# Optimization experiments

Hardware: AMD Instinct MI355X
Metric: run time of the kernel (lower is better)

## Reference

```python
import jax, jax.numpy as jnp
import numpy as np

B, T, D, H, LAT = 64, 512, 128, 512, 128


def setup_inputs() -> dict:
    key = jax.random.key(0)
    ks = jax.random.split(key, 17)
    s = lambda k, shape: (jax.random.normal(k, shape, jnp.float32) * 0.05)
    return {
        "padded_input": jax.random.normal(ks[0], (B, T, D), jnp.float32),
        "lengths": jnp.full((B,), T, jnp.int32),  # full lengths: packed == padded
        "W_ih_f": s(ks[1], (4 * H, D)), "W_hh_f": s(ks[2], (4 * H, H)), "b_f": s(ks[3], (4 * H,)),
        "W_ih_b": s(ks[4], (4 * H, D)), "W_hh_b": s(ks[5], (4 * H, H)), "b_b": s(ks[6], (4 * H,)),
        "W_ih_d": s(ks[7], (4 * H, D)), "W_hh_d": s(ks[8], (4 * H, H)), "b_d": s(ks[9], (4 * H,)),
        "W_lat": s(ks[10], (LAT, 4 * H)), "b_lat": s(ks[11], (LAT,)),
        "W_l2h": s(ks[12], (H, LAT)), "b_l2h": s(ks[13], (H,)),
        "W_out": s(ks[14], (D, H)), "b_out": s(ks[15], (D,)),
        "skip_alpha": jnp.asarray(0.5, jnp.float32),
    }


def _lstm(x, W_ih, W_hh, b, h0, c0):
    # x: [B, T, Din]; PyTorch gate order i, f, g, o; b = b_ih + b_hh pre-summed.
    xg = jnp.einsum('btd,gd->tbg', x, W_ih) + b  # [T, B, 4H], input GEMM hoisted out of scan

    def step(carry, xg_t):
        h, c = carry
        g = xg_t + h @ W_hh.T
        i, f, gc, o = jnp.split(g, 4, axis=-1)
        c = jax.nn.sigmoid(f) * c + jax.nn.sigmoid(i) * jnp.tanh(gc)
        h = jax.nn.sigmoid(o) * jnp.tanh(c)
        return (h, c), h

    (hT, cT), ys = jax.lax.scan(step, (h0, c0), xg)
    return jnp.transpose(ys, (1, 0, 2)), hT, cT  # [B, T, H], final h, final c


def reference(padded_input, lengths, W_ih_f, W_hh_f, b_f, W_ih_b, W_hh_b, b_b,
              W_ih_d, W_hh_d, b_d, W_lat, b_lat, W_l2h, b_l2h, W_out, b_out, skip_alpha):
    Bz, Tz, _ = padded_input.shape
    dt = padded_input.dtype
    z0 = jnp.zeros((Bz, H), dt)

    # Bidirectional encoder (single layer)
    out_f, hf, _ = _lstm(padded_input, W_ih_f, W_hh_f, b_f, z0, z0)
    out_b_rev, hb, _ = _lstm(padded_input[:, ::-1, :], W_ih_b, W_hh_b, b_b, z0, z0)
    out_b = out_b_rev[:, ::-1, :]
    enc_out = jnp.concatenate([out_f, out_b], axis=-1)  # [B, T, 2H]
    h_cat = jnp.concatenate([hf, hb], axis=-1)          # [B, 2H]

    # Masked mean pooling over valid timesteps
    mask = (jnp.arange(Tz)[None, :] < lengths[:, None]).astype(dt)[..., None]
    mean_hidden = (enc_out * mask).sum(axis=1) / lengths[:, None].astype(dt)
    latent_input = jnp.concatenate([h_cat, mean_hidden], axis=-1)  # [B, 4H]
    latent = latent_input @ W_lat.T + b_lat

    # Decoder init from latent; c0 = zeros
    h_dec = latent @ W_l2h.T + b_l2h

    # Teacher forcing with ratio 1.0, eval dropout, no noise:
    # per-step loop == one LSTM over padded_input[:, :T-1]
    dec_in = padded_input[:, :Tz - 1, :]
    y, _, _ = _lstm(dec_in, W_ih_d, W_hh_d, b_d, h_dec, jnp.zeros_like(h_dec))
    decoded = jnp.einsum('bth,dh->btd', y, W_out) + b_out  # [B, T-1, D]

    alpha = jax.nn.sigmoid(skip_alpha)
    return alpha * decoded + (1.0 - alpha) * padded_input[:, 1:, :]
```

## Files before the change

### kernel.cpp

```cpp
#include <hip/hip_runtime.h>
#include <cstdint>
#include <cstddef>

typedef __attribute__((ext_vector_type(8))) short bf16x8;
typedef __attribute__((ext_vector_type(4))) float f32x4;
typedef __attribute__((ext_vector_type(4))) unsigned u32x4;
typedef __attribute__((ext_vector_type(2))) unsigned u32x2;
typedef unsigned short ushort_t;

constexpr int kB = 64;
constexpr int kT = 512;
constexpr int kD = 128;
constexpr int kH = 512;
constexpr int kLat = 128;

constexpr size_t OFF_Y   = 0;
constexpr size_t Y_EL    = (size_t)(kT - 1) * kH * kB;
constexpr size_t OFF_XBF = OFF_Y + Y_EL;
constexpr size_t XBF_F   = (size_t)kT * kB * kD / 2;
constexpr size_t OFF_HT  = OFF_XBF + XBF_F;
constexpr size_t HT_F    = 3 * 2 * 32768 / 2;
constexpr size_t OFF_RDY = OFF_HT + HT_F;
constexpr size_t RDY_I   = 3 * 512 * 32;
constexpr size_t OFF_HFF = OFF_RDY + RDY_I;
constexpr size_t OFF_HFB = OFF_HFF + 32768;
constexpr size_t OFF_HSF = OFF_HFB + 32768;
constexpr size_t OFF_HSB = OFF_HSF + 32768;
constexpr size_t NEED_BYTES = (OFF_HSB + 32768) * 4;

#define MFMA_B16(A, Bv, C) C = __builtin_amdgcn_mfma_f32_16x16x32_bf16(A, Bv, C, 0, 0, 0)

__device__ __forceinline__ float sigf(float x) { return 1.0f / (1.0f + __expf(-x)); }
__device__ __forceinline__ float tanh_(float x) {
  float xc = fminf(fmaxf(x, -15.f), 15.f);
  float e = __expf(2.f * xc);
  return (e - 1.f) / (e + 1.f);
}
__device__ __forceinline__ ushort_t f2bf(float f) {
  unsigned u = __float_as_uint(f);
  u = (u + 0x7FFFu + ((u >> 16) & 1u)) >> 16;
  return (ushort_t)u;
}
__device__ __forceinline__ bf16x8 pack8(float4 a, float4 b) {
  bf16x8 v;
  v[0] = (short)f2bf(a.x); v[1] = (short)f2bf(a.y);
  v[2] = (short)f2bf(a.z); v[3] = (short)f2bf(a.w);
  v[4] = (short)f2bf(b.x); v[5] = (short)f2bf(b.y);
  v[6] = (short)f2bf(b.z); v[7] = (short)f2bf(b.w);
  return v;
}
__device__ __forceinline__ float cellup(const f32x4 a, float& c) {
  float ig = sigf(a[0]), fg = sigf(a[1]), gg = tanh_(a[2]), og = sigf(a[3]);
  c = fg * c + ig * gg;
  return og * tanh_(c);
}

__device__ __forceinline__ u32x4 llc_load_b128(const void* p) {
  u32x4 v;
  asm volatile("global_load_dwordx4 %0, %1, off sc0 sc1"
               : "=v"(v) : "v"(p) : "memory");
  return v;
}
__device__ __forceinline__ void llc_store_b64(void* p, u32x2 v) {
  asm volatile("global_store_dwordx2 %0, %1, off sc0 sc1"
               :: "v"(p), "v"(v) : "memory");
}
__device__ __forceinline__ void llc_store_b32(void* p, unsigned v) {
  asm volatile("global_store_dword %0, %1, off sc0 sc1"
               :: "v"(p), "v"(v) : "memory");
}
__device__ __forceinline__ void wait_vm0() {
  asm volatile("s_waitcnt vmcnt(0)" ::: "memory");
  __builtin_amdgcn_sched_barrier(0);
}

__global__ __launch_bounds__(256) void xbf_k(const float* __restrict__ X,
                                             ushort_t* __restrict__ xbf) {
  const int t = blockIdx.x, tid = threadIdx.x;
  const int b = tid >> 2, dq = (tid & 3) * 32;
  const float* src = X + ((size_t)b * kT + t) * kD + dq;
  ushort_t* dst = xbf + ((size_t)t * kB + b) * kD + dq;
  #pragma unroll
  for (int i = 0; i < 32; i += 8) {
    float4 u0 = *(const float4*)(src + i);
    float4 u1 = *(const float4*)(src + i + 4);
    *(bf16x8*)(dst + i) = pack8(u0, u1);
  }
}

__device__ __forceinline__ void xproj(const ushort_t* xb0, int q, const bf16x8* Ax,
                                      f32x4& a0, f32x4& a1, f32x4& a2, f32x4& a3,
                                      int b0n, int b1n, int b2n, int b3n) {
  #pragma unroll
  for (int ks = 0; ks < 4; ++ks) {
    const int ko = ks * 32 + q * 8;
    bf16x8 x0 = *(const bf16x8*)(xb0 + b0n * 128 + ko);
    bf16x8 x1 = *(const bf16x8*)(xb0 + b1n * 128 + ko);
    bf16x8 x2 = *(const bf16x8*)(xb0 + b2n * 128 + ko);
    bf16x8 x3 = *(const bf16x8*)(xb0 + b3n * 128 + ko);
    MFMA_B16(Ax[ks], x0, a0);
    MFMA_B16(Ax[ks], x1, a1);
    MFMA_B16(Ax[ks], x2, a2);
    MFMA_B16(Ax[ks], x3, a3);
  }
}

template<int MODE>
__global__ __launch_bounds__(256, 1) void lstm_k(
    const float* __restrict__ WhhA, const float* __restrict__ WhhB,
    const float* __restrict__ WihA, const float* __restrict__ WihB,
    const float* __restrict__ biaA, const float* __restrict__ biaB,
    const int* __restrict__ lengths, const ushort_t* __restrict__ xbf,
    float* __restrict__ ws) {
  __shared__ ushort_t hlds[32768];
  __shared__ ushort_t hx[64 * 20];
  const int tid = threadIdx.x;
  const int bid = blockIdx.x;
  const bool fwd = (MODE == 1) ? true : (bid < 32);
  const int gl = (MODE == 1) ? bid : (bid & 31);
  const float* Whh = fwd ? WhhA : WhhB;
  const float* Wih = fwd ? WihA : WihB;
  const float* bia = fwd ? biaA : biaB;
  const int dir_off = (MODE == 1) ? 2 : (fwd ? 0 : 1);
  ushort_t* hT = (ushort_t*)(ws + OFF_HT) + dir_off * 65536;
  unsigned* rdyf = (unsigned*)(ws + OFF_RDY) + (size_t)dir_off * 512 * 32;
  const int TS = (MODE == 1) ? (kT - 1) : kT;

  const int w = tid >> 6, lane = tid & 63;
  const int q = lane >> 4, r = lane & 15;
  const int JB = gl * 16;
  const int j4 = JB + 4 * w;
  const int gate = r & 3, jj = j4 + (r >> 2);

  bf16x8 Ah[16], Ax[4];
  {
    const float* p = Whh + ((size_t)(gate * kH + jj)) * kH + q * 8;
    #pragma unroll
    for (int ks = 0; ks < 16; ++ks)
      Ah[ks] = pack8(*(const float4*)(p + ks * 32), *(const float4*)(p + ks * 32 + 4));
    const float* px = Wih + ((size_t)(gate * kH + jj)) * kD + q * 8;
    #pragma unroll
    for (int ks = 0; ks < 4; ++ks)
      Ax[ks] = pack8(*(const float4*)(px + ks * 32), *(const float4*)(px + ks * 32 + 4));
  }
  const int jq = j4 + q;
  f32x4 bias_v;
  bias_v[0] = bia[0 * kH + jq];
  bias_v[1] = bia[1 * kH + jq];
  bias_v[2] = bia[2 * kH + jq];
  bias_v[3] = bia[3 * kH + jq];
  const int b0n = r, b1n = 16 + r, b2n = 32 + r, b3n = 48 + r;
  int len0 = 0, len1 = 0, len2 = 0, len3 = 0;
  if (MODE == 0) {
    len0 = lengths[b0n]; len1 = lengths[b1n];
    len2 = lengths[b2n]; len3 = lengths[b3n];
  }
  float c0 = 0.f, c1 = 0.f, c2 = 0.f, c3 = 0.f;
  float hs0 = 0.f, hs1 = 0.f, hs2 = 0.f, hs3 = 0.f;
  f32x4 a0 = bias_v, a1 = bias_v, a2 = bias_v, a3 = bias_v;
  {
    const int tx = fwd ? 0 : (kT - 1);
    xproj(xbf + (size_t)tx * 8192, q, Ax, a0, a1, a2, a3, b0n, b1n, b2n, b3n);
  }
  char* lp = (char*)hlds;
  float* yout = ws + OFF_Y;

  for (int t = 0; t < TS; ++t) {
    if (t > 0) {
      if (w == 0) {
        const unsigned* fp = rdyf + (size_t)t * 32 + (lane & 31);
        for (;;) {
          unsigned v = __hip_atomic_load(fp, __ATOMIC_RELAXED, __HIP_MEMORY_SCOPE_AGENT);
          if (__ballot(v != 0u) == ~0ull) break;
          __builtin_amdgcn_s_sleep(1);
        }
        __builtin_amdgcn_sched_barrier(0);
      }
      __syncthreads();
    }
    {
      const char* hsrc = (const char*)(hT + (t & 1) * 32768);
      u32x4 reg[16];
      #pragma unroll
      for (int i = 0; i < 16; ++i) {
        const int idx = tid + i * 256;
        reg[i] = llc_load_b128(hsrc + (size_t)idx * 16);
      }
      wait_vm0();
      #pragma unroll
      for (int i = 0; i < 16; ++i) {
        const int idx = tid + i * 256;
        const int bb = idx >> 6, cc = idx & 63;
        *(u32x4*)(lp + (((bb << 10) + (cc << 4)) ^ ((bb & 7) << 4))) = reg[i];
      }
    }
    __syncthreads();
    #pragma unroll
    for (int ks = 0; ks < 16; ++ks) {
      const int kb = ks * 64 + (q << 4);
      bf16x8 v0 = *(const bf16x8*)(lp + (((b0n << 10) + kb) ^ ((b0n & 7) << 4)));
      bf16x8 v1 = *(const bf16x8*)(lp + (((b1n << 10) + kb) ^ ((b1n & 7) << 4)));
      bf16x8 v2 = *(const bf16x8*)(lp + (((b2n << 10) + kb) ^ ((b2n & 7) << 4)));
      bf16x8 v3 = *(const bf16x8*)(lp + (((b3n << 10) + kb) ^ ((b3n & 7) << 4)));
      MFMA_B16(Ah[ks], v0, a0);
      MFMA_B16(Ah[ks], v1, a1);
      MFMA_B16(Ah[ks], v2, a2);
      MFMA_B16(Ah[ks], v3, a3);
    }
    const float h0v = cellup(a0, c0);
    const float h1v = cellup(a1, c1);
    const float h2v = cellup(a2, c2);
    const float h3v = cellup(a3, c3);
    if (MODE == 0) {
      const bool m0 = fwd ? (t < len0) : (t >= kT - len0);
      const bool m1 = fwd ? (t < len1) : (t >= kT - len1);
      const bool m2 = fwd ? (t < len2) : (t >= kT - len2);
      const bool m3 = fwd ? (t < len3) : (t >= kT - len3);
      hs0 += m0 ? h0v : 0.f;
      hs1 += m1 ? h1v : 0.f;
      hs2 += m2 ? h2v : 0.f;
      hs3 += m3 ? h3v : 0.f;
    } else {
      yout[((size_t)t * kH + jq) * kB + b0n] = h0v;
      yout[((size_t)t * kH + jq) * kB + b1n] = h1v;
      yout[((size_t)t * kH + jq) * kB + b2n] = h2v;
      yout[((size_t)t * kH + jq) * kB + b3n] = h3v;
    }
    if (t < TS - 1) {
      const int jl = 4 * w + q;
      hx[b0n * 20 + jl] = f2bf(h0v);
      hx[b1n * 20 + jl] = f2bf(h1v);
      hx[b2n * 20 + jl] = f2bf(h2v);
      hx[b3n * 20 + jl] = f2bf(h3v);
      __syncthreads();
      {
        const int bb = tid >> 2, c4 = (tid & 3) * 4;
        u32x2 v = *(const u32x2*)&hx[bb * 20 + c4];
        llc_store_b64(hT + ((t + 1) & 1) * 32768 + bb * 512 + JB + c4, v);
      }
      __syncthreads();
      if (tid == 0) llc_store_b32(rdyf + (size_t)(t + 1) * 32 + gl, 1u);
      a0 = bias_v; a1 = bias_v; a2 = bias_v; a3 = bias_v;
      const int tx = fwd ? (t + 1) : (kT - 1 - (t + 1));
      xproj(xbf + (size_t)tx * 8192, q, Ax, a0, a1, a2, a3, b0n, b1n, b2n, b3n);
    } else if (MODE == 0) {
      float* hfin = ws + (fwd ? OFF_HFF : OFF_HFB);
      float* hsum = ws + (fwd ? OFF_HSF : OFF_HSB);
      hfin[jq * kB + b0n] = h0v; hfin[jq * kB + b1n] = h1v;
      hfin[jq * kB + b2n] = h2v; hfin[jq * kB + b3n] = h3v;
      hsum[jq * kB + b0n] = hs0; hsum[jq * kB + b1n] = hs1;
      hsum[jq * kB + b2n] = hs2; hsum[jq * kB + b3n] = hs3;
    }
  }
}

__global__ __launch_bounds__(256) void latent_k(
    const float* __restrict__ W_lat, const float* __restrict__ b_lat,
    const float* __restrict__ W_l2h, const float* __restrict__ b_l2h,
    const int* __restrict__ lengths, float* __restrict__ ws) {
  __shared__ __align__(16) float li[4 * kH];
  __shared__ __align__(16) float ls[kLat];
  const int b = blockIdx.x;
  const int tid = threadIdx.x;
  const float invlen = 1.0f / (float)lengths[b];
  for (int j = tid; j < kH; j += 256) {
    li[j]          = ws[OFF_HFF + (size_t)j * kB + b];
    li[kH + j]     = ws[OFF_HFB + (size_t)j * kB + b];
    li[2 * kH + j] = ws[OFF_HSF + (size_t)j * kB + b] * invlen;
    li[3 * kH + j] = ws[OFF_HSB + (size_t)j * kB + b] * invlen;
  }
  __syncthreads();
  if (tid < kLat) {
    const float* wv = W_lat + (size_t)tid * (4 * kH);
    float a = b_lat[tid];
    for (int k = 0; k < 4 * kH; k += 4) {
      const float4 w4 = *(const float4*)(wv + k);
      a += w4.x * li[k] + w4.y * li[k + 1] + w4.z * li[k + 2] + w4.w * li[k + 3];
    }
    ls[tid] = a;
  }
  __syncthreads();
  ushort_t* hTd = (ushort_t*)(ws + OFF_HT) + 2 * 65536;
  for (int j = tid; j < kH; j += 256) {
    const float* wv = W_l2h + (size_t)j * kLat;
    float a = b_l2h[j];
    #pragma unroll
    for (int k = 0; k < kLat; k += 4) {
      const float4 w4 = *(const float4*)(wv + k);
      a += w4.x * ls[k] + w4.y * ls[k + 1] + w4.z * ls[k + 2] + w4.w * ls[k + 3];
    }
    hTd[b * kH + j] = f2bf(a);
  }
}

__global__ __launch_bounds__(256) void out_k(
    const float* __restrict__ X, const float* __restrict__ W_out,
    const float* __restrict__ b_out, const float* __restrict__ alpha_p,
    const float* __restrict__ ws, float* __restrict__ out) {
  __shared__ __align__(16) float ys[128 * 64];
  __shared__ __align__(16) float Wo[128 * 128];
  const int t = blockIdx.x;
  const float* y = ws + OFF_Y + (size_t)t * kH * kB;
  const int tid = threadIdx.x;
  float acc[8][4];
  #pragma unroll
  for (int i = 0; i < 8; ++i)
    #pragma unroll
    for (int jj = 0; jj < 4; ++jj) acc[i][jj] = 0.f;
  const int tg = tid >> 4, tb = tid & 15;
  const int d0 = tg * 8, b0 = tb * 4;
  for (int ch = 0; ch < 4; ++ch) {
    __syncthreads();
    {
      const float4* s4 = (const float4*)(y + ch * 128 * 64);
      float4* d4 = (float4*)ys;
      #pragma unroll
      for (int i = 0; i < 8; ++i) d4[tid + i * 256] = s4[tid + i * 256];
    }
    {
      const int d = tid & 127, k0 = (tid >> 7) * 64;
      const float* src = W_out + (size_t)d * kH + ch * 128 + k0;
      #pragma unroll
      for (int i = 0; i < 64; i += 4) {
        float4 v = *(const float4*)(src + i);
        Wo[(k0 + i + 0) * 128 + d] = v.x;
        Wo[(k0 + i + 1) * 128 + d] = v.y;
        Wo[(k0 + i + 2) * 128 + d] = v.z;
        Wo[(k0 + i + 3) * 128 + d] = v.w;
      }
    }
    __syncthreads();
    #pragma unroll 2
    for (int k = 0; k < 128; ++k) {
      const float4 yv = *(const float4*)&ys[k * 64 + b0];
      const float4 w0 = *(const float4*)&Wo[k * 128 + d0];
      const float4 w1 = *(const float4*)&Wo[k * 128 + d0 + 4];
      const float wv[8] = {w0.x, w0.y, w0.z, w0.w, w1.x, w1.y, w1.z, w1.w};
      const float ya[4] = {yv.x, yv.y, yv.z, yv.w};
      #pragma unroll
      for (int di = 0; di < 8; ++di)
        #pragma unroll
        for (int bi = 0; bi < 4; ++bi)
          acc[di][bi] += wv[di] * ya[bi];
    }
  }
  const float alpha = sigf(alpha_p[0]);
  const float beta = 1.0f - alpha;
  #pragma unroll
  for (int bi = 0; bi < 4; ++bi) {
    const int b = b0 + bi;
    const float* xrow = X + ((size_t)b * kT + t + 1) * kD + d0;
    float* orow = out + ((size_t)b * (kT - 1) + t) * kD + d0;
    #pragma unroll
    for (int di = 0; di < 8; di += 4) {
      const float4 xv = *(const float4*)(xrow + di);
      float4 o;
      o.x = alpha * (acc[di + 0][bi] + b_out[d0 + di + 0]) + beta * xv.x;
      o.y = alpha * (acc[di + 1][bi] + b_out[d0 + di + 1]) + beta * xv.y;
      o.z = alpha * (acc[di + 2][bi] + b_out[d0 + di + 2]) + beta * xv.z;
      o.w = alpha * (acc[di + 3][bi] + b_out[d0 + di + 3]) + beta * xv.w;
      *(float4*)(orow + di) = o;
    }
  }
}

__global__ __launch_bounds__(256) void fallback_k(
    const float* __restrict__ X, const float* __restrict__ alpha_p,
    float* __restrict__ out, int n) {
  const int o = blockIdx.x * 256 + threadIdx.x;
  if (o >= n) return;
  const float alpha = sigf(alpha_p[0]);
  const int b = o / ((kT - 1) * kD);
  const int rr = o % ((kT - 1) * kD);
  const int t = rr / kD, d = rr % kD;
  out[o] = (1.0f - alpha) * X[((size_t)b * kT + t + 1) * kD + d];
}

extern "C" void kernel_launch(void* const* d_in, const int* in_sizes, int n_in,
                              void* d_out, int out_size, void* d_ws, size_t ws_size,
                              hipStream_t stream) {
  const float* X      = (const float*)d_in[0];
  const int*   lens   = (const int*)  d_in[1];
  const float* W_ih_f = (const float*)d_in[2];
  const float* W_hh_f = (const float*)d_in[3];
  const float* b_f    = (const float*)d_in[4];
  const float* W_ih_b = (const float*)d_in[5];
  const float* W_hh_b = (const float*)d_in[6];
  const float* b_b    = (const float*)d_in[7];
  const float* W_ih_d = (const float*)d_in[8];
  const float* W_hh_d = (const float*)d_in[9];
  const float* b_d    = (const float*)d_in[10];
  const float* W_lat  = (const float*)d_in[11];
  const float* b_lat  = (const float*)d_in[12];
  const float* W_l2h  = (const float*)d_in[13];
  const float* b_l2h  = (const float*)d_in[14];
  const float* W_out  = (const float*)d_in[15];
  const float* b_out  = (const float*)d_in[16];
  const float* alpha  = (const float*)d_in[17];
  float* ws  = (float*)d_ws;
  float* out = (float*)d_out;

  if (ws_size < NEED_BYTES) {
    fallback_k<<<(out_size + 255) / 256, 256, 0, stream>>>(X, alpha, out, out_size);
    return;
  }

  hipMemsetAsync((void*)(ws + OFF_HT), 0, (HT_F + RDY_I) * sizeof(float), stream);

  ushort_t* xbf = (ushort_t*)(ws + OFF_XBF);
  xbf_k<<<kT, 256, 0, stream>>>(X, xbf);
  lstm_k<0><<<64, 256, 0, stream>>>(W_hh_f, W_hh_b, W_ih_f, W_ih_b, b_f, b_b,
                                    lens, xbf, ws);
  latent_k<<<64, 256, 0, stream>>>(W_lat, b_lat, W_l2h, b_l2h, lens, ws);
  lstm_k<1><<<32, 256, 0, stream>>>(W_hh_d, nullptr, W_ih_d, nullptr, b_d, nullptr,
                                    lens, xbf, ws);
  out_k<<<kT - 1, 256, 0, stream>>>(X, W_out, b_out, alpha, ws, out);
}
```

Before: 5.603 ms.

## Replace global barrier wait with per-producer flag polling and early h publish

Each wave now polls only the readiness flags of the 8 producer blocks whose hidden-state slice it consumes, and copies each slice into LDS as soon as that producer is ready. This replaces the single wave-0 wait on all 32 flags followed by a bulk copy. The new hidden state is also published before the mask/accumulate or y-store work rather than after it, shortening the cross-block critical path. The cost is more polling traffic, an extra __syncthreads before reusing the hx buffer, and more complex per-wave control flow.

```diff
diff --git a/kernel.cpp b/kernel.cpp
--- a/kernel.cpp
+++ b/kernel.cpp
@@ -164,53 +164,82 @@
   }
   char* lp = (char*)hlds;
   float* yout = ws + OFF_Y;
+  const int p0 = 8 * w;
 
   for (int t = 0; t < TS; ++t) {
-    if (t > 0) {
-      if (w == 0) {
-        const unsigned* fp = rdyf + (size_t)t * 32 + (lane & 31);
-        for (;;) {
-          unsigned v = __hip_atomic_load(fp, __ATOMIC_RELAXED, __HIP_MEMORY_SCOPE_AGENT);
-          if (__ballot(v != 0u) == ~0ull) break;
-          __builtin_amdgcn_s_sleep(1);
+    const bool do_rec = (MODE == 1) || (t > 0);
+    if (do_rec) {
+      const ushort_t* hbase = hT + (t & 1) * 32768;
+      unsigned done = 0;
+      while (done != 0xFFu) {
+        unsigned todo;
+        if (MODE == 0 || t > 0) {
+          unsigned fl = 0;
+          if (lane < 8)
+            fl = __hip_atomic_load(rdyf + (size_t)t * 32 + p0 + lane,
+                                   __ATOMIC_RELAXED, __HIP_MEMORY_SCOPE_AGENT);
+          unsigned rdy8 = (unsigned)(__ballot(fl != 0u) & 0xFFull);
+          todo = rdy8 & ~done;
+          if (!todo) { __builtin_amdgcn_s_sleep(1); continue; }
+          __builtin_amdgcn_sched_barrier(0);
+        } else {
+          todo = 0xFFu;
         }
-        __builtin_amdgcn_sched_barrier(0);
+        u32x4 r0v[8], r1v[8];
+        #pragma unroll
+        for (int pi = 0; pi < 8; ++pi) {
+          if ((todo >> pi) & 1u) {
+            const ushort_t* src = hbase + lane * 512 + (p0 + pi) * 16;
+            r0v[pi] = llc_load_b128(src);
+            r1v[pi] = llc_load_b128(src + 8);
+          }
+        }
+        wait_vm0();
+        #pragma unroll
+        for (int pi = 0; pi < 8; ++pi) {
+          if ((todo >> pi) & 1u) {
+            const int pb = (p0 + pi) << 5;
+            *(u32x4*)(lp + (((lane << 10) + pb) ^ ((lane & 7) << 4))) = r0v[pi];
+            *(u32x4*)(lp + (((lane << 10) + pb + 16) ^ ((lane & 7) << 4))) = r1v[pi];
+          }
+        }
+        done |= todo;
       }
       __syncthreads();
-    }
-    {
-      const char* hsrc = (const char*)(hT + (t & 1) * 32768);
-      u32x4 reg[16];
       #pragma unroll
-      for (int i = 0; i < 16; ++i) {
-        const int idx = tid + i * 256;
-        reg[i] = llc_load_b128(hsrc + (size_t)idx * 16);
+      for (int ks = 0; ks < 16; ++ks) {
+        const int kb = ks * 64 + (q << 4);
+        bf16x8 v0 = *(const bf16x8*)(lp + (((b0n << 10) + kb) ^ ((b0n & 7) << 4)));
+        bf16x8 v1 = *(const bf16x8*)(lp + (((b1n << 10) + kb) ^ ((b1n & 7) << 4)));
+        bf16x8 v2 = *(const bf16x8*)(lp + (((b2n << 10) + kb) ^ ((b2n & 7) << 4)));
+        bf16x8 v3 = *(const bf16x8*)(lp + (((b3n << 10) + kb) ^ ((b3n & 7) << 4)));
+        MFMA_B16(Ah[ks], v0, a0);
+        MFMA_B16(Ah[ks], v1, a1);
+        MFMA_B16(Ah[ks], v2, a2);
+        MFMA_B16(Ah[ks], v3, a3);
       }
-      wait_vm0();
-      #pragma unroll
-      for (int i = 0; i < 16; ++i) {
-        const int idx = tid + i * 256;
-        const int bb = idx >> 6, cc = idx & 63;
-        *(u32x4*)(lp + (((bb << 10) + (cc << 4)) ^ ((bb & 7) << 4))) = reg[i];
-      }
-    }
-    __syncthreads();
-    #pragma unroll
-    for (int ks = 0; ks < 16; ++ks) {
-      const int kb = ks * 64 + (q << 4);
-      bf16x8 v0 = *(const bf16x8*)(lp + (((b0n << 10) + kb) ^ ((b0n & 7) << 4)));
-      bf16x8 v1 = *(const bf16x8*)(lp + (((b1n << 10) + kb) ^ ((b1n & 7) << 4)));
-      bf16x8 v2 = *(const bf16x8*)(lp + (((b2n << 10) + kb) ^ ((b2n & 7) << 4)));
-      bf16x8 v3 = *(const bf16x8*)(lp + (((b3n << 10) + kb) ^ ((b3n & 7) << 4)));
-      MFMA_B16(Ah[ks], v0, a0);
-      MFMA_B16(Ah[ks], v1, a1);
-      MFMA_B16(Ah[ks], v2, a2);
-      MFMA_B16(Ah[ks], v3, a3);
     }
     const float h0v = cellup(a0, c0);
     const float h1v = cellup(a1, c1);
     const float h2v = cellup(a2, c2);
     const float h3v = cellup(a3, c3);
+
+    if (t < TS - 1) {
+      const int jl = 4 * w + q;
+      if (do_rec) __syncthreads();
+      hx[b0n * 20 + jl] = f2bf(h0v);
+      hx[b1n * 20 + jl] = f2bf(h1v);
+      hx[b2n * 20 + jl] = f2bf(h2v);
+      hx[b3n * 20 + jl] = f2bf(h3v);
+      __syncthreads();
+      {
+        const int bb = tid >> 2, c4 = (tid & 3) * 4;
+        u32x2 v = *(const u32x2*)&hx[bb * 20 + c4];
+        llc_store_b64(hT + ((t + 1) & 1) * 32768 + bb * 512 + JB + c4, v);
+      }
+      __syncthreads();
+      if (tid == 0) llc_store_b32(rdyf + (size_t)(t + 1) * 32 + gl, 1u);
+    }
     if (MODE == 0) {
       const bool m0 = fwd ? (t < len0) : (t >= kT - len0);
       const bool m1 = fwd ? (t < len1) : (t >= kT - len1);
@@ -227,19 +256,6 @@
       yout[((size_t)t * kH + jq) * kB + b3n] = h3v;
     }
     if (t < TS - 1) {
-      const int jl = 4 * w + q;
-      hx[b0n * 20 + jl] = f2bf(h0v);
-      hx[b1n * 20 + jl] = f2bf(h1v);
-      hx[b2n * 20 + jl] = f2bf(h2v);
-      hx[b3n * 20 + jl] = f2bf(h3v);
-      __syncthreads();
-      {
-        const int bb = tid >> 2, c4 = (tid & 3) * 4;
-        u32x2 v = *(const u32x2*)&hx[bb * 20 + c4];
-        llc_store_b64(hT + ((t + 1) & 1) * 32768 + bb * 512 + JB + c4, v);
-      }
-      __syncthreads();
-      if (tid == 0) llc_store_b32(rdyf + (size_t)(t + 1) * 32 + gl, 1u);
       a0 = bias_v; a1 = bias_v; a2 = bias_v; a3 = bias_v;
       const int tx = fwd ? (t + 1) : (kT - 1 - (t + 1));
       xproj(xbf + (size_t)tx * 8192, q, Ax, a0, a1, a2, a3, b0n, b1n, b2n, b3n);
```

Result: slower. 8.403 ms (+50.0%).

## Halve LSTM block count with 512-thread blocks and publish hidden state earlier

Applied to the files above, without the earlier changes.

The persistent LSTM kernels now use 16 blocks per direction of 512 threads each, with each block owning 32 hidden units instead of 16. The aim is to halve the number of blocks taking part in the per-step cross-block handshake and to spread the hidden-state copy over more threads. The new hidden state is also published, and its ready flag raised, before the masked-sum and output stores, so other blocks can start the next step sooner. The poll loop switches to inline-asm loads of only 16 flags. In exchange, each step does more work per block on fewer CUs, which serialises more of the recurrent compute.

```diff
diff --git a/kernel.cpp b/kernel.cpp
--- a/kernel.cpp
+++ b/kernel.cpp
@@ -13,6 +13,8 @@
 constexpr int kD = 128;
 constexpr int kH = 512;
 constexpr int kLat = 128;
+constexpr int kNP = 16;
+constexpr int kJW = 32;
 
 constexpr size_t OFF_Y   = 0;
 constexpr size_t Y_EL    = (size_t)(kT - 1) * kH * kB;
@@ -106,18 +108,18 @@
 }
 
 template<int MODE>
-__global__ __launch_bounds__(256, 1) void lstm_k(
+__global__ __launch_bounds__(512, 1) void lstm_k(
     const float* __restrict__ WhhA, const float* __restrict__ WhhB,
     const float* __restrict__ WihA, const float* __restrict__ WihB,
     const float* __restrict__ biaA, const float* __restrict__ biaB,
     const int* __restrict__ lengths, const ushort_t* __restrict__ xbf,
     float* __restrict__ ws) {
   __shared__ ushort_t hlds[32768];
-  __shared__ ushort_t hx[64 * 20];
+  __shared__ ushort_t hx[64 * 36];
   const int tid = threadIdx.x;
   const int bid = blockIdx.x;
-  const bool fwd = (MODE == 1) ? true : (bid < 32);
-  const int gl = (MODE == 1) ? bid : (bid & 31);
+  const bool fwd = (MODE == 1) ? true : (bid < kNP);
+  const int gl = (MODE == 1) ? bid : (bid & (kNP - 1));
   const float* Whh = fwd ? WhhA : WhhB;
   const float* Wih = fwd ? WihA : WihB;
   const float* bia = fwd ? biaA : biaB;
@@ -128,7 +130,7 @@
 
   const int w = tid >> 6, lane = tid & 63;
   const int q = lane >> 4, r = lane & 15;
-  const int JB = gl * 16;
+  const int JB = gl * kJW;
   const int j4 = JB + 4 * w;
   const int gate = r & 3, jj = j4 + (r >> 2);
 
@@ -159,58 +161,83 @@
   float hs0 = 0.f, hs1 = 0.f, hs2 = 0.f, hs3 = 0.f;
   f32x4 a0 = bias_v, a1 = bias_v, a2 = bias_v, a3 = bias_v;
   {
-    const int tx = fwd ? 0 : (kT - 1);
-    xproj(xbf + (size_t)tx * 8192, q, Ax, a0, a1, a2, a3, b0n, b1n, b2n, b3n);
+    const int tx0 = fwd ? 0 : (kT - 1);
+    xproj(xbf + (size_t)tx0 * 8192, q, Ax, a0, a1, a2, a3, b0n, b1n, b2n, b3n);
   }
   char* lp = (char*)hlds;
   float* yout = ws + OFF_Y;
 
   for (int t = 0; t < TS; ++t) {
-    if (t > 0) {
-      if (w == 0) {
-        const unsigned* fp = rdyf + (size_t)t * 32 + (lane & 31);
-        for (;;) {
-          unsigned v = __hip_atomic_load(fp, __ATOMIC_RELAXED, __HIP_MEMORY_SCOPE_AGENT);
-          if (__ballot(v != 0u) == ~0ull) break;
-          __builtin_amdgcn_s_sleep(1);
+    const bool do_rec = (MODE == 1) || (t > 0);
+    if (do_rec) {
+      if (t > 0) {
+        if (w == 0) {
+          const unsigned* fp = rdyf + (size_t)t * 32;
+          for (;;) {
+            unsigned fl = 1u;
+            if (lane < kNP) {
+              asm volatile("global_load_dword %0, %1, off sc0 sc1"
+                           : "=v"(fl) : "v"(fp + lane) : "memory");
+              asm volatile("s_waitcnt vmcnt(0)" ::: "memory");
+            }
+            if (__ballot(fl != 0u) == ~0ull) break;
+            __builtin_amdgcn_s_sleep(1);
+          }
+          __builtin_amdgcn_sched_barrier(0);
         }
-        __builtin_amdgcn_sched_barrier(0);
+        __syncthreads();
+      }
+      {
+        const char* hsrc = (const char*)(hT + (t & 1) * 32768);
+        u32x4 reg[8];
+        #pragma unroll
+        for (int i = 0; i < 8; ++i) {
+          const int idx = tid + i * 512;
+          reg[i] = llc_load_b128(hsrc + (size_t)idx * 16);
+        }
+        wait_vm0();
+        #pragma unroll
+        for (int i = 0; i < 8; ++i) {
+          const int idx = tid + i * 512;
+          const int bb = idx >> 6, cc = idx & 63;
+          *(u32x4*)(lp + (((bb << 10) + (cc << 4)) ^ ((bb & 7) << 4))) = reg[i];
+        }
       }
       __syncthreads();
-    }
-    {
-      const char* hsrc = (const char*)(hT + (t & 1) * 32768);
-      u32x4 reg[16];
       #pragma unroll
-      for (int i = 0; i < 16; ++i) {
-        const int idx = tid + i * 256;
-        reg[i] = llc_load_b128(hsrc + (size_t)idx * 16);
+      for (int ks = 0; ks < 16; ++ks) {
+        const int kb = ks * 64 + (q << 4);
+        bf16x8 v0 = *(const bf16x8*)(lp + (((b0n << 10) + kb) ^ ((b0n & 7) << 4)));
+        bf16x8 v1 = *(const bf16x8*)(lp + (((b1n << 10) + kb) ^ ((b1n & 7) << 4)));
+        bf16x8 v2 = *(const bf16x8*)(lp + (((b2n << 10) + kb) ^ ((b2n & 7) << 4)));
+        bf16x8 v3 = *(const bf16x8*)(lp + (((b3n << 10) + kb) ^ ((b3n & 7) << 4)));
+        MFMA_B16(Ah[ks], v0, a0);
+        MFMA_B16(Ah[ks], v1, a1);
+        MFMA_B16(Ah[ks], v2, a2);
+        MFMA_B16(Ah[ks], v3, a3);
       }
-      wait_vm0();
-      #pragma unroll
-      for (int i = 0; i < 16; ++i) {
-        const int idx = tid + i * 256;
-        const int bb = idx >> 6, cc = idx & 63;
-        *(u32x4*)(lp + (((bb << 10) + (cc << 4)) ^ ((bb & 7) << 4))) = reg[i];
-      }
-    }
-    __syncthreads();
-    #pragma unroll
-    for (int ks = 0; ks < 16; ++ks) {
-      const int kb = ks * 64 + (q << 4);
-      bf16x8 v0 = *(const bf16x8*)(lp + (((b0n << 10) + kb) ^ ((b0n & 7) << 4)));
-      bf16x8 v1 = *(const bf16x8*)(lp + (((b1n << 10) + kb) ^ ((b1n & 7) << 4)));
-      bf16x8 v2 = *(const bf16x8*)(lp + (((b2n << 10) + kb) ^ ((b2n & 7) << 4)));
-      bf16x8 v3 = *(const bf16x8*)(lp + (((b3n << 10) + kb) ^ ((b3n & 7) << 4)));
-      MFMA_B16(Ah[ks], v0, a0);
-      MFMA_B16(Ah[ks], v1, a1);
-      MFMA_B16(Ah[ks], v2, a2);
-      MFMA_B16(Ah[ks], v3, a3);
     }
     const float h0v = cellup(a0, c0);
     const float h1v = cellup(a1, c1);
     const float h2v = cellup(a2, c2);
     const float h3v = cellup(a3, c3);
+
+    if (t < TS - 1) {
+      const int jl = 4 * w + q;
+      if (do_rec) __syncthreads();
+      hx[b0n * 36 + jl] = f2bf(h0v);
+      hx[b1n * 36 + jl] = f2bf(h1v);
+      hx[b2n * 36 + jl] = f2bf(h2v);
+      hx[b3n * 36 + jl] = f2bf(h3v);
+      __syncthreads();
+      {
+        const int bb = tid >> 3, c4 = (tid & 7) * 4;
+        u32x2 v = *(const u32x2*)&hx[bb * 36 + c4];
+        llc_store_b64(hT + ((t + 1) & 1) * 32768 + bb * 512 + JB + c4, v);
+      }
+      __syncthreads();
+      if (tid == 0) llc_store_b32(rdyf + (size_t)(t + 1) * 32 + gl, 1u);
+    }
     if (MODE == 0) {
       const bool m0 = fwd ? (t < len0) : (t >= kT - len0);
       const bool m1 = fwd ? (t < len1) : (t >= kT - len1);
@@ -227,22 +254,9 @@
       yout[((size_t)t * kH + jq) * kB + b3n] = h3v;
     }
     if (t < TS - 1) {
-      const int jl = 4 * w + q;
-      hx[b0n * 20 + jl] = f2bf(h0v);
-      hx[b1n * 20 + jl] = f2bf(h1v);
-      hx[b2n * 20 + jl] = f2bf(h2v);
-      hx[b3n * 20 + jl] = f2bf(h3v);
-      __syncthreads();
-      {
-        const int bb = tid >> 2, c4 = (tid & 3) * 4;
-        u32x2 v = *(const u32x2*)&hx[bb * 20 + c4];
-        llc_store_b64(hT + ((t + 1) & 1) * 32768 + bb * 512 + JB + c4, v);
-      }
-      __syncthreads();
-      if (tid == 0) llc_store_b32(rdyf + (size_t)(t + 1) * 32 + gl, 1u);
       a0 = bias_v; a1 = bias_v; a2 = bias_v; a3 = bias_v;
-      const int tx = fwd ? (t + 1) : (kT - 1 - (t + 1));
-      xproj(xbf + (size_t)tx * 8192, q, Ax, a0, a1, a2, a3, b0n, b1n, b2n, b3n);
+      const int txn = fwd ? (t + 1) : (kT - 1 - (t + 1));
+      xproj(xbf + (size_t)txn * 8192, q, Ax, a0, a1, a2, a3, b0n, b1n, b2n, b3n);
     } else if (MODE == 0) {
       float* hfin = ws + (fwd ? OFF_HFF : OFF_HFB);
       float* hsum = ws + (fwd ? OFF_HSF : OFF_HSB);
@@ -409,10 +423,10 @@
 
   ushort_t* xbf = (ushort_t*)(ws + OFF_XBF);
   xbf_k<<<kT, 256, 0, stream>>>(X, xbf);
-  lstm_k<0><<<64, 256, 0, stream>>>(W_hh_f, W_hh_b, W_ih_f, W_ih_b, b_f, b_b,
-                                    lens, xbf, ws);
+  lstm_k<0><<<2 * kNP, 512, 0, stream>>>(W_hh_f, W_hh_b, W_ih_f, W_ih_b, b_f, b_b,
+                                         lens, xbf, ws);
   latent_k<<<64, 256, 0, stream>>>(W_lat, b_lat, W_l2h, b_l2h, lens, ws);
-  lstm_k<1><<<32, 256, 0, stream>>>(W_hh_d, nullptr, W_ih_d, nullptr, b_d, nullptr,
-                                    lens, xbf, ws);
+  lstm_k<1><<<kNP, 512, 0, stream>>>(W_hh_d, nullptr, W_ih_d, nullptr, b_d, nullptr,
+                                     lens, xbf, ws);
   out_k<<<kT - 1, 256, 0, stream>>>(X, W_out, b_out, alpha, ws, out);
 }
```

Result: slower. 8.563 ms (+52.8%).
